# Performance work log

Hardware: AMD Instinct MI355X
Metric: run time of the kernel (lower is better)

## Reference

```python
import jax, jax.numpy as jnp
import numpy as np

N, G, D = 50000, 1024, 512


def _ff(x, w0, b0, w1, b1, w2, b2, ws, bs):
    h = jax.nn.relu(x @ w0.T + b0)
    h = jax.nn.relu(h @ w1.T + b1)
    h = jax.nn.relu(h @ w2.T + b2)
    return h + x @ ws.T + bs


def setup_inputs() -> dict:
    key = jax.random.key(0)
    ks = jax.random.split(key, 20)
    s = 1.0 / np.sqrt(D)  # xavier-ish scale
    def W(k):
        return jax.random.normal(k, (D, D), dtype=jnp.float32) * s
    inp = {
        "node_rep": jax.random.normal(ks[0], (N, D), dtype=jnp.float32),
        "graph_rep": jax.random.normal(ks[1], (G, D), dtype=jnp.float32),
        "batch": jnp.sort(jax.random.randint(ks[2], (N,), 0, G)),
    }
    names = ["lw0", "lw1", "lw2", "lws", "gw0", "gw1", "gw2", "gws"]
    for i, nm in enumerate(names):
        inp[nm] = W(ks[3 + i])
        inp[nm.replace("w", "b")] = jnp.zeros((D,), dtype=jnp.float32)
    return inp


def reference(node_rep, graph_rep, batch,
              lw0, lb0, lw1, lb1, lw2, lb2, lws, lbs,
              gw0, gb0, gw1, gb1, gw2, gb2, gws, gbs):
    l_enc = _ff(node_rep, lw0, lb0, lw1, lb1, lw2, lb2, lws, lbs)   # [N, D]
    g_enc = _ff(graph_rep, gw0, gb0, gw1, gb1, gw2, gb2, gws, gbs)  # [G, D]
    num_nodes = l_enc.shape[0]
    num_graphs = g_enc.shape[0]
    log2 = jnp.log(jnp.float32(2.0))

    pos_mask = jax.nn.one_hot(batch, num_graphs, dtype=l_enc.dtype)  # [N, G]
    neg_mask = 1.0 - pos_mask

    res = l_enc @ g_enc.T  # [N, G]

    # JSD positive expectation: log(2) - softplus(-p)
    p = res * pos_mask
    E_pos = (log2 - jax.nn.softplus(-p)).sum() / num_nodes
    # JSD negative expectation: softplus(-q) + q - log(2)
    q = res * neg_mask
    E_neg = (jax.nn.softplus(-q) + q - log2).sum() / (num_nodes * (num_graphs - 1))
    return E_neg - E_pos
```

## Files before the change

kernel.cpp:

```cpp
#include <hip/hip_runtime.h>
#include <hip/hip_bf16.h>

#define N_NODE  50000
#define N_PAD   50048
#define N_GRAPH 1024
#define DD      512
#define NK8     8
#define NJSD    3128

typedef __attribute__((ext_vector_type(4))) float f32x4;
typedef __attribute__((ext_vector_type(2))) long long ll2;

__device__ __forceinline__ unsigned char f2fp8(float f) {
  unsigned int u = __builtin_bit_cast(unsigned int, f);
  unsigned int sg = (u >> 24) & 0x80u;
  float a = __builtin_bit_cast(float, u & 0x7fffffffu);
  a = fminf(a, 448.0f);
  unsigned int r = __builtin_bit_cast(unsigned int, a);
  unsigned int rn = r + 0x7ffffu + ((r >> 20) & 1u);
  int codeN = (int)(rn >> 20) - (120 << 3);
  int codeS = (int)rintf(a * 512.0f);
  int code = (a >= 0.015625f) ? codeN : codeS;
  code = code > 0x7E ? 0x7E : code;
  return (unsigned char)(sg | (unsigned int)code);
}

__device__ __forceinline__ long long permute_col(long long c) {
  int o = (int)c & 63;
  int p = (((o >> 3) & 3) << 4) | ((o >> 5) << 3) | (o & 7);
  return (c & ~63LL) | p;
}

__device__ __forceinline__ void gload16(const void* g, void* l) {
  __builtin_amdgcn_global_load_lds(
      (const __attribute__((address_space(1))) unsigned int*)g,
      (__attribute__((address_space(3))) unsigned int*)l, 16, 0, 0);
}

__device__ __forceinline__ int xcd_remap(int bid, int nwg) {
  int xcd = bid & 7;
  int local = bid >> 3;
  int q = nwg >> 3, r = nwg & 7;
  int base = (xcd < r) ? xcd * (q + 1) : r * (q + 1) + (xcd - r) * q;
  return base + local;
}


__global__ void cast_pad8_kernel(const float* __restrict__ src,
                                 unsigned char* __restrict__ dst,
                                 int srcRows, int dstRows) {
  long long base = ((long long)blockIdx.x * blockDim.x + threadIdx.x) * 8;
  if (base >= (long long)dstRows * DD) return;
  int row = (int)(base >> 9);
  unsigned long long pk = 0ULL;
  if (row < srcRows) {
    float4 x0 = reinterpret_cast<const float4*>(src + base)[0];
    float4 x1 = reinterpret_cast<const float4*>(src + base)[1];
    pk  = (unsigned long long)f2fp8(x0.x);
    pk |= (unsigned long long)f2fp8(x0.y) << 8;
    pk |= (unsigned long long)f2fp8(x0.z) << 16;
    pk |= (unsigned long long)f2fp8(x0.w) << 24;
    pk |= (unsigned long long)f2fp8(x1.x) << 32;
    pk |= (unsigned long long)f2fp8(x1.y) << 40;
    pk |= (unsigned long long)f2fp8(x1.z) << 48;
    pk |= (unsigned long long)f2fp8(x1.w) << 56;
  }
  *reinterpret_cast<unsigned long long*>(dst + permute_col(base)) = pk;
}

struct WPtrs { const float* p[8]; };

__global__ void cast_w8_kernel(WPtrs ps, unsigned char* __restrict__ dst) {
  long long base = ((long long)blockIdx.x * blockDim.x + threadIdx.x) * 8;
  int mat = (int)(base >> 18);
  long long off = base & 262143LL;
  const float* s = ps.p[mat] + off;
  float4 x0 = reinterpret_cast<const float4*>(s)[0];
  float4 x1 = reinterpret_cast<const float4*>(s)[1];
  unsigned long long pk;
  pk  = (unsigned long long)f2fp8(x0.x);
  pk |= (unsigned long long)f2fp8(x0.y) << 8;
  pk |= (unsigned long long)f2fp8(x0.z) << 16;
  pk |= (unsigned long long)f2fp8(x0.w) << 24;
  pk |= (unsigned long long)f2fp8(x1.x) << 32;
  pk |= (unsigned long long)f2fp8(x1.y) << 40;
  pk |= (unsigned long long)f2fp8(x1.z) << 48;
  pk |= (unsigned long long)f2fp8(x1.w) << 56;
  *reinterpret_cast<unsigned long long*>(
      dst + (long long)mat * 262144 + permute_col(off)) = pk;
}

__global__ void zeropad8_kernel(unsigned char* __restrict__ H) {
  long long i = (long long)blockIdx.x * blockDim.x + threadIdx.x;
  long long base = (long long)N_NODE * DD + i * 16;
  if (base < (long long)N_PAD * DD) {
    int4 z = {0, 0, 0, 0};
    *reinterpret_cast<int4*>(H + base) = z;
  }
}


__device__ __forceinline__ void ff_stage(const unsigned char* aptr,
                                         const unsigned char* bptr, int kbyte,
                                         unsigned char* sA, unsigned char* sB,
                                         int wid) {
  unsigned char* dA = sA + wid * 1024;
  unsigned char* dB = sB + wid * 1024;
  gload16(aptr + kbyte, dA);
  gload16(aptr + 64LL * DD + kbyte, dA + 4096);
  gload16(bptr + kbyte, dB);
  gload16(bptr + 64LL * DD + kbyte, dB + 4096);
}

__device__ __forceinline__ void gemm_core128_fp8(
    const unsigned char* aptr, const unsigned char* bptr,
    unsigned char* As, unsigned char* Bs,
    int wid, int rA, int rB, int offs, f32x4 acc[4][4]) {
  ff_stage(aptr, bptr, 0, As, Bs, wid);
  ff_stage(aptr, bptr, 64, As + 8192, Bs + 8192, wid);
  ff_stage(aptr, bptr, 128, As + 16384, Bs + 16384, wid);
  #pragma unroll
  for (int t = 0; t < NK8; ++t) {
    __builtin_amdgcn_sched_barrier(0);
    if (t < NK8 - 2)       asm volatile("s_waitcnt vmcnt(8)" ::: "memory");
    else if (t == NK8 - 2) asm volatile("s_waitcnt vmcnt(4)" ::: "memory");
    else                   asm volatile("s_waitcnt vmcnt(0)" ::: "memory");
    __builtin_amdgcn_s_barrier();
    __builtin_amdgcn_sched_barrier(0);
    if (t + 3 < NK8)
      ff_stage(aptr, bptr, (t + 3) * 64, As + ((t + 3) & 3) * 8192,
               Bs + ((t + 3) & 3) * 8192, wid);
    const unsigned char* as = As + (t & 3) * 8192;
    const unsigned char* bs = Bs + (t & 3) * 8192;
    ll2 a[4], b[4];
    #pragma unroll
    for (int m = 0; m < 4; ++m)
      a[m] = *reinterpret_cast<const ll2*>(as + (rA + m * 16) * 64 + offs);
    #pragma unroll
    for (int n = 0; n < 4; ++n)
      b[n] = *reinterpret_cast<const ll2*>(bs + (rB + n * 16) * 64 + offs);
    __builtin_amdgcn_s_setprio(1);
    #pragma unroll
    for (int m = 0; m < 4; ++m)
      #pragma unroll
      for (int n = 0; n < 4; ++n)
        acc[m][n] = __builtin_amdgcn_mfma_f32_16x16x32_fp8_fp8(a[m][0], b[n][0], acc[m][n], 0, 0, 0);
    #pragma unroll
    for (int m = 0; m < 4; ++m)
      #pragma unroll
      for (int n = 0; n < 4; ++n)
        acc[m][n] = __builtin_amdgcn_mfma_f32_16x16x32_fp8_fp8(a[m][1], b[n][1], acc[m][n], 0, 0, 0);
    __builtin_amdgcn_s_setprio(0);
  }
}


template <int DUAL>
__global__ __launch_bounds__(256, 2) void gemm_ff8(
    const unsigned char* __restrict__ Al, const unsigned char* __restrict__ Wl,
    const float* __restrict__ biasl, unsigned char* __restrict__ Cl,
    const unsigned char* __restrict__ A2l, const unsigned char* __restrict__ W2l,
    const float* __restrict__ bias2l, int nwgL,
    const unsigned char* __restrict__ Ag, const unsigned char* __restrict__ Wg,
    const float* __restrict__ biasg, unsigned char* __restrict__ Cg,
    const unsigned char* __restrict__ A2g, const unsigned char* __restrict__ W2g,
    const float* __restrict__ bias2g) {
  __shared__ unsigned char As[4 * 8192];
  __shared__ unsigned char Bs[4 * 8192];
  const int tid = threadIdx.x;
  const int lane = tid & 63, wid = tid >> 6;
  const int wr = wid >> 1, wc = wid & 1;

  int tile = xcd_remap(blockIdx.x, gridDim.x);
  const unsigned char *A, *W, *A2, *W2;
  const float *bias, *bias2;
  unsigned char* C;
  if (tile < nwgL) {
    A = Al; W = Wl; bias = biasl; C = Cl; A2 = A2l; W2 = W2l; bias2 = bias2l;
  } else {
    tile -= nwgL;
    A = Ag; W = Wg; bias = biasg; C = Cg; A2 = A2g; W2 = W2g; bias2 = bias2g;
  }
  const long long brow = (long long)(tile >> 2) * 128;
  const long long bcol = (long long)(tile & 3) * 128;

  const int r0 = (tid >> 6) * 16 + ((tid & 63) >> 2);
  const int csrc = (((tid & 3) ^ ((r0 >> 1) & 3))) * 16;
  const unsigned char* aptr = A + (brow + r0) * DD + csrc;
  const unsigned char* bptr = W + (bcol + r0) * DD + csrc;

  const int rA = wr * 64 + (lane & 15);
  const int rB = wc * 64 + (lane & 15);
  const int offs = (((lane >> 4) ^ (((lane & 15) >> 1) & 3)) << 4);

  f32x4 acc[4][4];
  f32x4 zero = {0.f, 0.f, 0.f, 0.f};
  #pragma unroll
  for (int m = 0; m < 4; ++m)
    #pragma unroll
    for (int n = 0; n < 4; ++n) acc[m][n] = zero;

  gemm_core128_fp8(aptr, bptr, As, Bs, wid, rA, rB, offs, acc);

  float bv[4];
  #pragma unroll
  for (int n = 0; n < 4; ++n) bv[n] = bias[bcol + wc * 64 + n * 16 + (lane & 15)];

  if constexpr (DUAL) {
    float r[4][4][4];
    #pragma unroll
    for (int m = 0; m < 4; ++m)
      #pragma unroll
      for (int n = 0; n < 4; ++n)
        #pragma unroll
        for (int j = 0; j < 4; ++j)
          r[m][n][j] = fmaxf(acc[m][n][j] + bv[n], 0.f);
    #pragma unroll
    for (int m = 0; m < 4; ++m)
      #pragma unroll
      for (int n = 0; n < 4; ++n) acc[m][n] = zero;

    const unsigned char* aptr2 = A2 + (brow + r0) * DD + csrc;
    const unsigned char* bptr2 = W2 + (bcol + r0) * DD + csrc;
    gemm_core128_fp8(aptr2, bptr2, As, Bs, wid, rA, rB, offs, acc);

    float b2[4];
    #pragma unroll
    for (int n = 0; n < 4; ++n) b2[n] = bias2[bcol + wc * 64 + n * 16 + (lane & 15)];

    #pragma unroll
    for (int m = 0; m < 4; ++m) {
      const long long row = brow + wr * 64 + m * 16 + (lane >> 4) * 4;
      #pragma unroll
      for (int j = 0; j < 4; ++j)
        #pragma unroll
        for (int n = 0; n < 4; ++n) {
          const long long col = bcol + wc * 64 + n * 16 + (lane & 15);
          float v = r[m][n][j] + acc[m][n][j] + b2[n];
          C[(row + j) * DD + permute_col(col)] = f2fp8(v);
        }
    }
  } else {
    #pragma unroll
    for (int m = 0; m < 4; ++m) {
      const long long row = brow + wr * 64 + m * 16 + (lane >> 4) * 4;
      #pragma unroll
      for (int j = 0; j < 4; ++j)
        #pragma unroll
        for (int n = 0; n < 4; ++n) {
          const long long col = bcol + wc * 64 + n * 16 + (lane & 15);
          float v = fmaxf(acc[m][n][j] + bv[n], 0.f);
          C[(row + j) * DD + permute_col(col)] = f2fp8(v);
        }
    }
  }
}


__global__ __launch_bounds__(256, 2) void gemm_jsd128(
    const unsigned char* __restrict__ A, const unsigned char* __restrict__ B,
    const int* __restrict__ batch, float* __restrict__ parts) {
  __shared__ unsigned char As[4 * 8192];
  __shared__ unsigned char Bs[4 * 8192];
  __shared__ int sbatch[128];
  __shared__ float sred[12];
  const int tid = threadIdx.x;
  const int lane = tid & 63, wid = tid >> 6;
  const int wr = wid >> 1, wc = wid & 1;

  const int tile = xcd_remap(blockIdx.x, gridDim.x);
  const long long brow = (long long)(tile >> 3) * 128;
  const long long bcol = (long long)(tile & 7) * 128;

  if (tid < 128) {
    long long gr = brow + tid;
    sbatch[tid] = (gr < N_NODE) ? batch[gr] : -1;
  }

  const int r0 = (tid >> 6) * 16 + ((tid & 63) >> 2);
  const int csrc = (((tid & 3) ^ ((r0 >> 1) & 3))) * 16;
  const unsigned char* aptr = A + (brow + r0) * DD + csrc;
  const unsigned char* bptr = B + (bcol + r0) * DD + csrc;

  const int rA = wr * 64 + (lane & 15);
  const int rB = wc * 64 + (lane & 15);
  const int offs = (((lane >> 4) ^ (((lane & 15) >> 1) & 3)) << 4);

  f32x4 acc[4][4];
  f32x4 zero = {0.f, 0.f, 0.f, 0.f};
  #pragma unroll
  for (int m = 0; m < 4; ++m)
    #pragma unroll
    for (int n = 0; n < 4; ++n) acc[m][n] = zero;

  gemm_core128_fp8(aptr, bptr, As, Bs, wid, rA, rB, offs, acc);

  const float LN2 = 0.69314718055994530942f;
  float sAll = 0.f, sPos = 0.f, sDiag = 0.f;
  #pragma unroll
  for (int m = 0; m < 4; ++m) {
    #pragma unroll
    for (int j = 0; j < 4; ++j) {
      const int lr = wr * 64 + m * 16 + (lane >> 4) * 4 + j;
      const int bg = sbatch[lr];
      #pragma unroll
      for (int n = 0; n < 4; ++n) {
        const int col = (int)bcol + wc * 64 + n * 16 + (lane & 15);
        float v = acc[m][n][j];
        float t = __expf(-fabsf(v));
        float spn = fmaxf(-v, 0.f) + __logf(1.0f + t);
        sAll += spn + v;
        if (col == bg) {
          sPos += LN2 - spn;
          sDiag += spn + v;
        }
      }
    }
  }
  #pragma unroll
  for (int off = 32; off > 0; off >>= 1) {
    sAll  += __shfl_down(sAll, off);
    sPos  += __shfl_down(sPos, off);
    sDiag += __shfl_down(sDiag, off);
  }
  if (lane == 0) { sred[wid] = sPos; sred[4 + wid] = sAll; sred[8 + wid] = sDiag; }
  __syncthreads();
  if (tid == 0) {
    float* o = parts + 3 * blockIdx.x;
    o[0] = sred[0] + sred[1] + sred[2] + sred[3];
    o[1] = sred[4] + sred[5] + sred[6] + sred[7];
    o[2] = sred[8] + sred[9] + sred[10] + sred[11];
  }
}


__global__ __launch_bounds__(1024) void reduce_finalize(
    const float* __restrict__ parts, float* __restrict__ out) {
  __shared__ double sp[16], sa[16], sd[16];
  const int tid = threadIdx.x;
  double p = 0.0, a = 0.0, d = 0.0;
  for (int i = tid; i < NJSD; i += 1024) {
    p += (double)parts[3 * i];
    a += (double)parts[3 * i + 1];
    d += (double)parts[3 * i + 2];
  }
  #pragma unroll
  for (int off = 32; off > 0; off >>= 1) {
    p += __shfl_down(p, off);
    a += __shfl_down(a, off);
    d += __shfl_down(d, off);
  }
  const int lane = tid & 63, wid = tid >> 6;
  if (lane == 0) { sp[wid] = p; sa[wid] = a; sd[wid] = d; }
  __syncthreads();
  if (tid == 0) {
    double P = 0.0, Aa = 0.0, Dd = 0.0;
    #pragma unroll
    for (int w = 0; w < 16; ++w) { P += sp[w]; Aa += sa[w]; Dd += sd[w]; }
    const double LN2 = 0.6931471805599453094172321;
    double negSum = (Aa - Dd) - ((double)N_PAD * N_GRAPH - (double)N_NODE) * LN2;
    double Epos = P / (double)N_NODE;
    double Eneg = negSum / ((double)N_NODE * (double)(N_GRAPH - 1));
    out[0] = (float)(Eneg - Epos);
  }
}


extern "C" void kernel_launch(void* const* d_in, const int* in_sizes, int n_in,
                              void* d_out, int out_size, void* d_ws, size_t ws_size,
                              hipStream_t stream) {
  const float* node  = (const float*)d_in[0];
  const float* graph = (const float*)d_in[1];
  const int*   batch = (const int*)d_in[2];
  const float* lw0 = (const float*)d_in[3];
  const float* lb0 = (const float*)d_in[4];
  const float* lw1 = (const float*)d_in[5];
  const float* lb1 = (const float*)d_in[6];
  const float* lw2 = (const float*)d_in[7];
  const float* lb2 = (const float*)d_in[8];
  const float* lws = (const float*)d_in[9];
  const float* lbs = (const float*)d_in[10];
  const float* gw0 = (const float*)d_in[11];
  const float* gb0 = (const float*)d_in[12];
  const float* gw1 = (const float*)d_in[13];
  const float* gb1 = (const float*)d_in[14];
  const float* gw2 = (const float*)d_in[15];
  const float* gb2 = (const float*)d_in[16];
  const float* gws = (const float*)d_in[17];
  const float* gbs = (const float*)d_in[18];

  char* ws = (char*)d_ws;
  unsigned char* WB8   = (unsigned char*)(ws + 256);
  float*         parts = (float*)(ws + 2097408LL);
  unsigned char* XB8   = (unsigned char*)(ws + 4194560LL);
  unsigned char* H1_8  = (unsigned char*)(ws + 55443712LL);
  unsigned char* H2_8  = (unsigned char*)(ws + 106692864LL);
  unsigned char* GXB8  = (unsigned char*)(ws + 157942016LL);
  unsigned char* GH18  = (unsigned char*)(ws + 158990592LL);
  unsigned char* GH28  = (unsigned char*)(ws + 160039168LL);
  if (ws_size < 161087744ULL) return;

  WPtrs wp;
  wp.p[0] = lw0; wp.p[1] = lw1; wp.p[2] = lw2; wp.p[3] = lws;
  wp.p[4] = gw0; wp.p[5] = gw1; wp.p[6] = gw2; wp.p[7] = gws;
  cast_w8_kernel<<<1024, 256, 0, stream>>>(wp, WB8);
  cast_pad8_kernel<<<12512, 256, 0, stream>>>(node, XB8, N_NODE, N_PAD);
  cast_pad8_kernel<<<256, 256, 0, stream>>>(graph, GXB8, N_GRAPH, N_GRAPH);

  dim3 blk256(256);
  const int nwgL = 4 * 391;
  const int nwgG = 4 * 8;
  dim3 gff(nwgL + nwgG);

  gemm_ff8<0><<<gff, blk256, 0, stream>>>(
      XB8, WB8 + 0 * 262144, lb0, H1_8, nullptr, nullptr, nullptr, nwgL,
      GXB8, WB8 + 4 * 262144, gb0, GH18, nullptr, nullptr, nullptr);
  gemm_ff8<0><<<gff, blk256, 0, stream>>>(
      H1_8, WB8 + 1 * 262144, lb1, H2_8, nullptr, nullptr, nullptr, nwgL,
      GH18, WB8 + 5 * 262144, gb1, GH28, nullptr, nullptr, nullptr);
  gemm_ff8<1><<<gff, blk256, 0, stream>>>(
      H2_8, WB8 + 2 * 262144, lb2, H1_8, XB8, WB8 + 3 * 262144, lbs, nwgL,
      GH28, WB8 + 6 * 262144, gb2, GH18, GXB8, WB8 + 7 * 262144, gbs);

  zeropad8_kernel<<<6, 256, 0, stream>>>(H1_8);

  dim3 gr(NJSD);
  gemm_jsd128<<<gr, blk256, 0, stream>>>(H1_8, GH18, batch, parts);
  reduce_finalize<<<1, 1024, 0, stream>>>(parts, (float*)d_out);
}
```

Measured before the change: 221.8 us.

## Load B operand directly from global into registers, bypassing LDS staging

The GEMM core now stages only the A tile through LDS with async global-to-LDS loads. Each wave reads its B fragments straight from global memory into registers with dwordx4 loads every k-step, and the vmcnt waits are retuned to match. This halves LDS use and drops the min-blocks-per-CU launch bound, aiming to cut LDS traffic and barrier pressure. In exchange, B loads are not prefetched, so their global latency sits inside each iteration. Waves that share B columns also fetch the same data redundantly from L2.

```diff
diff --git a/kernel.cpp b/kernel.cpp
--- a/kernel.cpp
+++ b/kernel.cpp
@@ -35,6 +35,12 @@
   __builtin_amdgcn_global_load_lds(
       (const __attribute__((address_space(1))) unsigned int*)g,
       (__attribute__((address_space(3))) unsigned int*)l, 16, 0, 0);
+}
+
+__device__ __forceinline__ ll2 gldB(const unsigned char* p) {
+  ll2 r;
+  asm volatile("global_load_dwordx4 %0, %1, off" : "=v"(r) : "v"(p));
+  return r;
 }
 
 __device__ __forceinline__ int xcd_remap(int bid, int nwg) {
@@ -100,45 +106,42 @@
 }
 
 
-__device__ __forceinline__ void ff_stage(const unsigned char* aptr,
-                                         const unsigned char* bptr, int kbyte,
-                                         unsigned char* sA, unsigned char* sB,
-                                         int wid) {
+struct BP4 { const unsigned char* p[4]; };
+
+__device__ __forceinline__ void stageA(const unsigned char* aptr, int kbyte,
+                                       unsigned char* sA, int wid) {
   unsigned char* dA = sA + wid * 1024;
-  unsigned char* dB = sB + wid * 1024;
   gload16(aptr + kbyte, dA);
   gload16(aptr + 64LL * DD + kbyte, dA + 4096);
-  gload16(bptr + kbyte, dB);
-  gload16(bptr + 64LL * DD + kbyte, dB + 4096);
-}
-
-__device__ __forceinline__ void gemm_core128_fp8(
-    const unsigned char* aptr, const unsigned char* bptr,
-    unsigned char* As, unsigned char* Bs,
-    int wid, int rA, int rB, int offs, f32x4 acc[4][4]) {
-  ff_stage(aptr, bptr, 0, As, Bs, wid);
-  ff_stage(aptr, bptr, 64, As + 8192, Bs + 8192, wid);
-  ff_stage(aptr, bptr, 128, As + 16384, Bs + 16384, wid);
+}
+
+__device__ __forceinline__ void gemm_core128_bd(
+    const unsigned char* aptr, const BP4& bp,
+    unsigned char* As, int wid, int rA, int offsA, f32x4 acc[4][4]) {
+  stageA(aptr, 0, As, wid);
+  stageA(aptr, 64, As + 8192, wid);
+  stageA(aptr, 128, As + 16384, wid);
+  asm volatile("s_waitcnt vmcnt(4)" ::: "memory");
+  __builtin_amdgcn_sched_barrier(0);
+  __builtin_amdgcn_s_barrier();
   #pragma unroll
   for (int t = 0; t < NK8; ++t) {
-    __builtin_amdgcn_sched_barrier(0);
-    if (t < NK8 - 2)       asm volatile("s_waitcnt vmcnt(8)" ::: "memory");
-    else if (t == NK8 - 2) asm volatile("s_waitcnt vmcnt(4)" ::: "memory");
-    else                   asm volatile("s_waitcnt vmcnt(0)" ::: "memory");
-    __builtin_amdgcn_s_barrier();
+    if (t) __builtin_amdgcn_s_barrier();
+    ll2 b[4];
+    #pragma unroll
+    for (int n = 0; n < 4; ++n) b[n] = gldB(bp.p[n] + t * 64);
     __builtin_amdgcn_sched_barrier(0);
     if (t + 3 < NK8)
-      ff_stage(aptr, bptr, (t + 3) * 64, As + ((t + 3) & 3) * 8192,
-               Bs + ((t + 3) & 3) * 8192, wid);
+      stageA(aptr, (t + 3) * 64, As + ((t + 3) & 3) * 8192, wid);
+    __builtin_amdgcn_sched_barrier(0);
     const unsigned char* as = As + (t & 3) * 8192;
-    const unsigned char* bs = Bs + (t & 3) * 8192;
-    ll2 a[4], b[4];
+    ll2 a[4];
     #pragma unroll
     for (int m = 0; m < 4; ++m)
-      a[m] = *reinterpret_cast<const ll2*>(as + (rA + m * 16) * 64 + offs);
-    #pragma unroll
-    for (int n = 0; n < 4; ++n)
-      b[n] = *reinterpret_cast<const ll2*>(bs + (rB + n * 16) * 64 + offs);
+      a[m] = *reinterpret_cast<const ll2*>(as + (rA + m * 16) * 64 + offsA);
+    if (t + 3 < NK8) asm volatile("s_waitcnt vmcnt(2)" ::: "memory");
+    else             asm volatile("s_waitcnt vmcnt(0)" ::: "memory");
+    __builtin_amdgcn_sched_barrier(0);
     __builtin_amdgcn_s_setprio(1);
     #pragma unroll
     for (int m = 0; m < 4; ++m)
@@ -156,7 +159,7 @@
 
 
 template <int DUAL>
-__global__ __launch_bounds__(256, 2) void gemm_ff8(
+__global__ __launch_bounds__(256) void gemm_ff8(
     const unsigned char* __restrict__ Al, const unsigned char* __restrict__ Wl,
     const float* __restrict__ biasl, unsigned char* __restrict__ Cl,
     const unsigned char* __restrict__ A2l, const unsigned char* __restrict__ W2l,
@@ -166,7 +169,6 @@
     const unsigned char* __restrict__ A2g, const unsigned char* __restrict__ W2g,
     const float* __restrict__ bias2g) {
   __shared__ unsigned char As[4 * 8192];
-  __shared__ unsigned char Bs[4 * 8192];
   const int tid = threadIdx.x;
   const int lane = tid & 63, wid = tid >> 6;
   const int wr = wid >> 1, wc = wid & 1;
@@ -187,11 +189,16 @@
   const int r0 = (tid >> 6) * 16 + ((tid & 63) >> 2);
   const int csrc = (((tid & 3) ^ ((r0 >> 1) & 3))) * 16;
   const unsigned char* aptr = A + (brow + r0) * DD + csrc;
-  const unsigned char* bptr = W + (bcol + r0) * DD + csrc;
 
   const int rA = wr * 64 + (lane & 15);
-  const int rB = wc * 64 + (lane & 15);
-  const int offs = (((lane >> 4) ^ (((lane & 15) >> 1) & 3)) << 4);
+  const int rBl = wc * 64 + (lane & 15);
+  const int qa16 = (lane >> 4) * 16;
+  const int offsA = (((lane >> 4) ^ (((lane & 15) >> 1) & 3)) << 4);
+
+  BP4 bp;
+  #pragma unroll
+  for (int n = 0; n < 4; ++n)
+    bp.p[n] = W + (bcol + rBl + n * 16) * DD + qa16;
 
   f32x4 acc[4][4];
   f32x4 zero = {0.f, 0.f, 0.f, 0.f};
@@ -200,7 +207,7 @@
     #pragma unroll
     for (int n = 0; n < 4; ++n) acc[m][n] = zero;
 
-  gemm_core128_fp8(aptr, bptr, As, Bs, wid, rA, rB, offs, acc);
+  gemm_core128_bd(aptr, bp, As, wid, rA, offsA, acc);
 
   float bv[4];
   #pragma unroll
@@ -221,8 +228,11 @@
       for (int n = 0; n < 4; ++n) acc[m][n] = zero;
 
     const unsigned char* aptr2 = A2 + (brow + r0) * DD + csrc;
-    const unsigned char* bptr2 = W2 + (bcol + r0) * DD + csrc;
-    gemm_core128_fp8(aptr2, bptr2, As, Bs, wid, rA, rB, offs, acc);
+    BP4 bp2;
+    #pragma unroll
+    for (int n = 0; n < 4; ++n)
+      bp2.p[n] = W2 + (bcol + rBl + n * 16) * DD + qa16;
+    gemm_core128_bd(aptr2, bp2, As, wid, rA, offsA, acc);
 
     float b2[4];
     #pragma unroll
@@ -257,11 +267,10 @@
 }
 
 
-__global__ __launch_bounds__(256, 2) void gemm_jsd128(
+__global__ __launch_bounds__(256) void gemm_jsd128(
     const unsigned char* __restrict__ A, const unsigned char* __restrict__ B,
     const int* __restrict__ batch, float* __restrict__ parts) {
   __shared__ unsigned char As[4 * 8192];
-  __shared__ unsigned char Bs[4 * 8192];
   __shared__ int sbatch[128];
   __shared__ float sred[12];
   const int tid = threadIdx.x;
@@ -280,11 +289,16 @@
   const int r0 = (tid >> 6) * 16 + ((tid & 63) >> 2);
   const int csrc = (((tid & 3) ^ ((r0 >> 1) & 3))) * 16;
   const unsigned char* aptr = A + (brow + r0) * DD + csrc;
-  const unsigned char* bptr = B + (bcol + r0) * DD + csrc;
 
   const int rA = wr * 64 + (lane & 15);
-  const int rB = wc * 64 + (lane & 15);
-  const int offs = (((lane >> 4) ^ (((lane & 15) >> 1) & 3)) << 4);
+  const int rBl = wc * 64 + (lane & 15);
+  const int qa16 = (lane >> 4) * 16;
+  const int offsA = (((lane >> 4) ^ (((lane & 15) >> 1) & 3)) << 4);
+
+  BP4 bp;
+  #pragma unroll
+  for (int n = 0; n < 4; ++n)
+    bp.p[n] = B + (bcol + rBl + n * 16) * DD + qa16;
 
   f32x4 acc[4][4];
   f32x4 zero = {0.f, 0.f, 0.f, 0.f};
@@ -293,7 +307,7 @@
     #pragma unroll
     for (int n = 0; n < 4; ++n) acc[m][n] = zero;
 
-  gemm_core128_fp8(aptr, bptr, As, Bs, wid, rA, rB, offs, acc);
+  gemm_core128_bd(aptr, bp, As, wid, rA, offsA, acc);
 
   const float LN2 = 0.69314718055994530942f;
   float sAll = 0.f, sPos = 0.f, sDiag = 0.f;
```

Result: slower. 276.1 us (+24.5%).
